# Optimization experiments

Measured on AMD Instinct MI355X. Metric: run time of the kernel, lower is better.

## Reference

```python
import jax, jax.numpy as jnp
import numpy as np

N_DOMAIN, D_IN, UNITS, LORA_R = 64, 256, 128, 4
BATCH = 131072


def setup_inputs() -> dict:
    key = jax.random.key(0)
    ks = jax.random.split(key, 7)
    x = jax.random.normal(ks[0], (BATCH, D_IN), dtype=jnp.float32)
    domain_indicator = jax.random.randint(ks[1], (BATCH, 1), 0, N_DOMAIN, dtype=jnp.int32)
    a_kernel = jax.random.normal(ks[2], (N_DOMAIN, D_IN, LORA_R), dtype=jnp.float32) * 0.05
    b_kernel = jax.random.normal(ks[3], (N_DOMAIN, LORA_R, UNITS), dtype=jnp.float32) * 0.05
    domain_bias = jax.random.normal(ks[4], (N_DOMAIN, UNITS), dtype=jnp.float32) * 0.05
    kernel = jax.random.normal(ks[5], (D_IN, UNITS), dtype=jnp.float32) * 0.05
    bias = jax.random.normal(ks[6], (UNITS,), dtype=jnp.float32) * 0.05
    return {"x": x, "domain_indicator": domain_indicator, "a_kernel": a_kernel,
            "b_kernel": b_kernel, "domain_bias": domain_bias, "kernel": kernel, "bias": bias}


def reference(x, domain_indicator, a_kernel, b_kernel, domain_bias, kernel, bias):
    # shared dense path (dropout is identity at inference)
    out = x @ kernel + bias  # [B, units]
    # domain index: original uses domain_indicator[0, 0] (one domain per batch)
    idx = domain_indicator[0, 0]
    A = a_kernel[idx]        # [d_in, r]
    B = b_kernel[idx]        # [r, units]
    db = domain_bias[idx]    # [units]
    out = out + (x @ A) @ B + db
    return jax.nn.relu(out)
```

## Files before the change

### kernel.cpp

```cpp
#include <hip/hip_runtime.h>
#include <hip/hip_bf16.h>

#define D_IN   256
#define UNITS  128
#define LORA_R 4
#define ROWS_PER_TILE   16
#define TILES_PER_BLOCK 4
#define GRID_GEMM       2048

typedef __attribute__((ext_vector_type(8))) short short8;
typedef __attribute__((ext_vector_type(4))) float f32x4;

#define BARRIER()  asm volatile("s_barrier" ::: "memory")
#define VMCNT(n)   asm volatile("s_waitcnt vmcnt(" #n ")" ::: "memory")

static __device__ __forceinline__ unsigned short f2bf(float f) {
    unsigned u = __float_as_uint(f);
    unsigned r = (u + 0x7FFFu + ((u >> 16) & 1u)) >> 16;
    return (unsigned short)r;
}

static __device__ __forceinline__ void gll16(const void* g, void* l) {
    __builtin_amdgcn_global_load_lds(
        (const __attribute__((address_space(1))) unsigned int*)g,
        (__attribute__((address_space(3))) unsigned int*)l,
        16, 0, 0);
}

__global__ void mlora_prep(const float* __restrict__ a_kernel,
                           const float* __restrict__ b_kernel,
                           const float* __restrict__ domain_bias,
                           const float* __restrict__ kernel,
                           const float* __restrict__ bias,
                           const int* __restrict__ dom,
                           unsigned short* __restrict__ wfrag,
                           float* __restrict__ bias_eff) {
    const int idx = dom[0];
    const int tid = blockIdx.x * 256 + threadIdx.x;
    const int n = tid & (UNITS - 1);
    const int k = tid >> 7;
    const float* __restrict__ A = a_kernel + (size_t)idx * D_IN * LORA_R;
    const float* __restrict__ B = b_kernel + (size_t)idx * LORA_R * UNITS;
    float w = kernel[k * UNITS + n];
#pragma unroll
    for (int r = 0; r < LORA_R; ++r) w += A[k * LORA_R + r] * B[r * UNITS + n];
    const int s = k >> 5, g = (k >> 3) & 3, j = k & 7;
    const int t = n >> 4, lo = n & 15;
    const int lane = g * 16 + lo;
    wfrag[(size_t)((s * 8 + t) * 64 + lane) * 8 + j] = f2bf(w);
    if (tid < UNITS) bias_eff[tid] = bias[tid] + domain_bias[idx * UNITS + tid];
}

__global__ __launch_bounds__(256, 4) void mlora_gemm(
    const float* __restrict__ x,
    const unsigned short* __restrict__ wfrag,
    const float* __restrict__ bias_eff,
    float* __restrict__ out) {
    __shared__ float lds[2][ROWS_PER_TILE * 256];
    const int lane = threadIdx.x & 63;
    const int wave = threadIdx.x >> 6;
    const int t0 = wave * 2;
    const int rlo = lane & 15;
    const int g = lane >> 4;

    short8 bfrag[8][2];
#pragma unroll
    for (int s = 0; s < 8; ++s) {
#pragma unroll
        for (int tt = 0; tt < 2; ++tt) {
            bfrag[s][tt] = *reinterpret_cast<const short8*>(
                wfrag + (size_t)((s * 8 + t0 + tt) * 64 + lane) * 8);
        }
    }
    const float b0 = bias_eff[t0 * 16 + rlo];
    const float b1 = bias_eff[(t0 + 1) * 16 + rlo];

    const size_t block_row0 = (size_t)blockIdx.x * (ROWS_PER_TILE * TILES_PER_BLOCK);
    const int swz = (rlo & 7) << 4;

    auto stage = [&](int bufi, int tile) {
        const char* gbase = (const char*)x +
            (block_row0 + (size_t)tile * ROWS_PER_TILE + wave * 4) * 1024;
        char* lbase = (char*)&lds[bufi][0] + (size_t)wave * 4 * 1024;
#pragma unroll
        for (int i = 0; i < 4; ++i) {
            const int rsw = (wave * 4 + i) & 7;
            gll16(gbase + (size_t)i * 1024 + ((lane * 16) ^ (rsw << 4)),
                  lbase + (size_t)i * 1024);
        }
    };

    auto compute_tile = [&](int bufi, int tile) {
        const size_t r0g = block_row0 + (size_t)tile * ROWS_PER_TILE;
        const char* lrow = (const char*)&lds[bufi][0] + (size_t)rlo * 1024;
        f32x4 acc0 = {0.f, 0.f, 0.f, 0.f};
        f32x4 acc1 = {0.f, 0.f, 0.f, 0.f};
#pragma unroll
        for (int s = 0; s < 8; ++s) {
            const int base = s * 128 + g * 32;
            f32x4 u0 = *reinterpret_cast<const f32x4*>(lrow + (base ^ swz));
            f32x4 u1 = *reinterpret_cast<const f32x4*>(lrow + ((base + 16) ^ swz));
            union { short8 s8; __hip_bfloat162 h2[4]; } af;
            af.h2[0] = __float22bfloat162_rn(make_float2(u0[0], u0[1]));
            af.h2[1] = __float22bfloat162_rn(make_float2(u0[2], u0[3]));
            af.h2[2] = __float22bfloat162_rn(make_float2(u1[0], u1[1]));
            af.h2[3] = __float22bfloat162_rn(make_float2(u1[2], u1[3]));
            acc0 = __builtin_amdgcn_mfma_f32_16x16x32_bf16(af.s8, bfrag[s][0], acc0, 0, 0, 0);
            acc1 = __builtin_amdgcn_mfma_f32_16x16x32_bf16(af.s8, bfrag[s][1], acc1, 0, 0, 0);
        }
        float* op = out + (r0g + g * 4) * UNITS;
#pragma unroll
        for (int j = 0; j < 4; ++j) {
            op[(size_t)j * UNITS + t0 * 16 + rlo]      = fmaxf(acc0[j] + b0, 0.f);
            op[(size_t)j * UNITS + t0 * 16 + 16 + rlo] = fmaxf(acc1[j] + b1, 0.f);
        }
    };

    stage(0, 0);

    stage(1, 1);
    VMCNT(4);
    BARRIER();
    compute_tile(0, 0);
    BARRIER();
    stage(0, 2);
    VMCNT(12);
    BARRIER();
    compute_tile(1, 1);
    BARRIER();
    stage(1, 3);
    VMCNT(12);
    BARRIER();
    compute_tile(0, 2);
    BARRIER();
    VMCNT(8);
    BARRIER();
    compute_tile(1, 3);
}

extern "C" void kernel_launch(void* const* d_in, const int* in_sizes, int n_in,
                              void* d_out, int out_size, void* d_ws, size_t ws_size,
                              hipStream_t stream) {
    const float* x           = (const float*)d_in[0];
    const int*   dom         = (const int*)d_in[1];
    const float* a_kernel    = (const float*)d_in[2];
    const float* b_kernel    = (const float*)d_in[3];
    const float* domain_bias = (const float*)d_in[4];
    const float* kernel      = (const float*)d_in[5];
    const float* bias        = (const float*)d_in[6];
    float* out = (float*)d_out;

    unsigned short* wfrag = (unsigned short*)d_ws;
    float* bias_eff = (float*)((char*)d_ws + 65536);

    mlora_prep<<<128, 256, 0, stream>>>(a_kernel, b_kernel, domain_bias,
                                        kernel, bias, dom, wfrag, bias_eff);
    mlora_gemm<<<GRID_GEMM, 256, 0, stream>>>(x, wfrag, bias_eff, out);
}
```

Baseline: 40.63 us.

## Fuse weight-merge prep into GEMM kernel and double tiles per block

Drops the separate prep kernel. Each GEMM block now builds its own bf16 B fragments straight from kernel + A@B and computes the effective bias in registers, which removes one launch and the workspace round trip. To spread the duplicated merge work over more rows, each block handles 8 tiles instead of 4 and the grid is halved. The cost is redundant weight reads and FMAs in every block (1024 blocks each read the 128KB fp32 kernel, mostly from cache), plus a longer per-block prologue before streaming x starts.

```diff
diff --git a/kernel.cpp b/kernel.cpp
--- a/kernel.cpp
+++ b/kernel.cpp
@@ -5,8 +5,8 @@
 #define UNITS  128
 #define LORA_R 4
 #define ROWS_PER_TILE   16
-#define TILES_PER_BLOCK 4
-#define GRID_GEMM       2048
+#define TILES_PER_BLOCK 8
+#define GRID_GEMM       1024
 
 typedef __attribute__((ext_vector_type(8))) short short8;
 typedef __attribute__((ext_vector_type(4))) float f32x4;
@@ -27,34 +27,14 @@
         16, 0, 0);
 }
 
-__global__ void mlora_prep(const float* __restrict__ a_kernel,
-                           const float* __restrict__ b_kernel,
-                           const float* __restrict__ domain_bias,
-                           const float* __restrict__ kernel,
-                           const float* __restrict__ bias,
-                           const int* __restrict__ dom,
-                           unsigned short* __restrict__ wfrag,
-                           float* __restrict__ bias_eff) {
-    const int idx = dom[0];
-    const int tid = blockIdx.x * 256 + threadIdx.x;
-    const int n = tid & (UNITS - 1);
-    const int k = tid >> 7;
-    const float* __restrict__ A = a_kernel + (size_t)idx * D_IN * LORA_R;
-    const float* __restrict__ B = b_kernel + (size_t)idx * LORA_R * UNITS;
-    float w = kernel[k * UNITS + n];
-#pragma unroll
-    for (int r = 0; r < LORA_R; ++r) w += A[k * LORA_R + r] * B[r * UNITS + n];
-    const int s = k >> 5, g = (k >> 3) & 3, j = k & 7;
-    const int t = n >> 4, lo = n & 15;
-    const int lane = g * 16 + lo;
-    wfrag[(size_t)((s * 8 + t) * 64 + lane) * 8 + j] = f2bf(w);
-    if (tid < UNITS) bias_eff[tid] = bias[tid] + domain_bias[idx * UNITS + tid];
-}
-
-__global__ __launch_bounds__(256, 4) void mlora_gemm(
+__global__ __launch_bounds__(256, 4) void mlora_fused(
     const float* __restrict__ x,
-    const unsigned short* __restrict__ wfrag,
-    const float* __restrict__ bias_eff,
+    const int*   __restrict__ dom,
+    const float* __restrict__ a_kernel,
+    const float* __restrict__ b_kernel,
+    const float* __restrict__ domain_bias,
+    const float* __restrict__ kernel,
+    const float* __restrict__ bias,
     float* __restrict__ out) {
     __shared__ float lds[2][ROWS_PER_TILE * 256];
     const int lane = threadIdx.x & 63;
@@ -63,17 +43,41 @@
     const int rlo = lane & 15;
     const int g = lane >> 4;
 
+    const int idx = dom[0];
+    const float* __restrict__ A = a_kernel + (size_t)idx * D_IN * LORA_R;
+    const float* __restrict__ Bm = b_kernel + (size_t)idx * LORA_R * UNITS;
+
+    const int c0 = t0 * 16 + rlo, c1 = c0 + 16;
+    const float b0 = bias[c0] + domain_bias[(size_t)idx * UNITS + c0];
+    const float b1 = bias[c1] + domain_bias[(size_t)idx * UNITS + c1];
+
+    float bv[2][4];
+#pragma unroll
+    for (int tt = 0; tt < 2; ++tt) {
+        const int n = c0 + tt * 16;
+#pragma unroll
+        for (int r = 0; r < 4; ++r) bv[tt][r] = Bm[r * UNITS + n];
+    }
     short8 bfrag[8][2];
 #pragma unroll
     for (int s = 0; s < 8; ++s) {
+        const int k0 = s * 32 + g * 8;
 #pragma unroll
         for (int tt = 0; tt < 2; ++tt) {
-            bfrag[s][tt] = *reinterpret_cast<const short8*>(
-                wfrag + (size_t)((s * 8 + t0 + tt) * 64 + lane) * 8);
+            const int n = c0 + tt * 16;
+            union { short8 s8; unsigned short u[8]; } w;
+#pragma unroll
+            for (int j = 0; j < 8; ++j) {
+                const int k = k0 + j;
+                const float* __restrict__ ap = A + (size_t)k * 4;
+                float wv = kernel[(size_t)k * UNITS + n]
+                         + ap[0] * bv[tt][0] + ap[1] * bv[tt][1]
+                         + ap[2] * bv[tt][2] + ap[3] * bv[tt][3];
+                w.u[j] = f2bf(wv);
+            }
+            bfrag[s][tt] = w.s8;
         }
     }
-    const float b0 = bias_eff[t0 * 16 + rlo];
-    const float b1 = bias_eff[(t0 + 1) * 16 + rlo];
 
     const size_t block_row0 = (size_t)blockIdx.x * (ROWS_PER_TILE * TILES_PER_BLOCK);
     const int swz = (rlo & 7) << 4;
@@ -117,25 +121,22 @@
     };
 
     stage(0, 0);
-
     stage(1, 1);
     VMCNT(4);
     BARRIER();
     compute_tile(0, 0);
     BARRIER();
-    stage(0, 2);
-    VMCNT(12);
-    BARRIER();
-    compute_tile(1, 1);
-    BARRIER();
-    stage(1, 3);
-    VMCNT(12);
-    BARRIER();
-    compute_tile(0, 2);
-    BARRIER();
+#pragma unroll
+    for (int t = 1; t < 7; ++t) {
+        stage((t + 1) & 1, t + 1);
+        VMCNT(12);
+        BARRIER();
+        compute_tile(t & 1, t);
+        BARRIER();
+    }
     VMCNT(8);
     BARRIER();
-    compute_tile(1, 3);
+    compute_tile(1, 7);
 }
 
 extern "C" void kernel_launch(void* const* d_in, const int* in_sizes, int n_in,
@@ -149,11 +150,8 @@
     const float* kernel      = (const float*)d_in[5];
     const float* bias        = (const float*)d_in[6];
     float* out = (float*)d_out;
+    (void)d_ws; (void)ws_size;
 
-    unsigned short* wfrag = (unsigned short*)d_ws;
-    float* bias_eff = (float*)((char*)d_ws + 65536);
-
-    mlora_prep<<<128, 256, 0, stream>>>(a_kernel, b_kernel, domain_bias,
-                                        kernel, bias, dom, wfrag, bias_eff);
-    mlora_gemm<<<GRID_GEMM, 256, 0, stream>>>(x, wfrag, bias_eff, out);
+    mlora_fused<<<GRID_GEMM, 256, 0, stream>>>(x, dom, a_kernel, b_kernel,
+                                               domain_bias, kernel, bias, out);
 }
```

Measured after the change: 100.4 us. 147% more time.
